# Optimization experiments

Hardware: AMD Instinct MI355X
Metric: run time of the kernel (lower is better)

Reference implementation:

```python
import jax, jax.numpy as jnp
import numpy as np

N_NEIGHBORS = 9
MIN_STD, MAX_STD = 0.01, 0.5
EPS_NORM = 1e-8


def setup_inputs() -> dict:
    key = jax.random.key(0)
    k1, k2, k3 = jax.random.split(key, 3)
    B, C, H, W = 8, 1024, 28, 28
    M, D = 16384, 1024
    features = jax.random.normal(k1, (B, C, H, W), dtype=jnp.float32)
    memory_bank = jax.random.normal(k2, (M, D), dtype=jnp.float32)
    influence_weight = jnp.ones((D,), dtype=jnp.float32)
    distance_weight = jnp.ones((1,), dtype=jnp.float32)
    eps = jax.random.normal(k3, (B * H * W, D), dtype=jnp.float32)  # randn_like noise
    return {"features": features, "memory_bank": memory_bank,
            "influence_weight": influence_weight, "distance_weight": distance_weight,
            "eps": eps}


def reference(features, memory_bank, influence_weight, distance_weight, eps):
    B, C, H, W = features.shape
    M, D = memory_bank.shape
    x = features.transpose(0, 2, 3, 1).reshape(B * H * W, C)  # [N, D]
    N = x.shape[0]

    d2 = (jnp.sum(x * x, axis=1, keepdims=True)
          + jnp.sum(memory_bank * memory_bank, axis=1)[None, :]
          - 2.0 * (x @ memory_bank.T))  # [N, M]
    dist = jnp.sqrt(jnp.clip(d2, 1e-12))

    k = min(N_NEIGHBORS, M)
    neg_topd, idx = jax.lax.top_k(-dist, k)  # smallest-k distances
    topk_distances = -neg_topd  # [N, k]

    # Per-dimension influence: mean |x - nn| over k neighbors, scaled by weight
    nn_feats = memory_bank[idx]  # [N, k, D] gather
    influence = jnp.abs(x[:, None, :] - nn_feats).mean(axis=1) * influence_weight[None, :]  # [N, D]

    # Row-wise normalization (torch std is unbiased, ddof=1)
    infl_norm = ((influence - influence.mean(axis=-1, keepdims=True))
                 / (jnp.std(influence, axis=-1, ddof=1, keepdims=True) + EPS_NORM))

    # Distance signal: per-row mean distance, normalized by global stats of the
    # [N, D]-expanded tensor (each row value repeated D times -> same mean,
    # unbiased std uses N*D - 1 in the denominator).
    ds = topk_distances.mean(axis=-1, keepdims=True)  # [N, 1]
    full_mean = ds.mean()
    full_std = jnp.sqrt(jnp.sum((ds - full_mean) ** 2) * D / (N * D - 1))
    dist_norm = (ds - full_mean) / (full_std + EPS_NORM)  # [N, 1], broadcasts over D

    combined = infl_norm + distance_weight * dist_norm  # [N, D]
    noise_std = MIN_STD + (MAX_STD - MIN_STD) * jax.nn.sigmoid(combined)

    noised = (x + eps * noise_std).reshape(B, H, W, C).transpose(0, 3, 1, 2)
    influence_map = influence.mean(axis=-1).reshape(B, H, W)
    noise_std_map = noise_std.mean(axis=-1).reshape(B, H, W)
    return noised, influence_map, noise_std_map
```

## Files before the change

kernel.cpp:

```cpp
#include <hip/hip_runtime.h>
#include <hip/hip_bf16.h>
#include <stdint.h>

#define N_ROWS 6272
#define DIM    1024
#define M_ROWS 16384
#define KNN    9
#define BMS    128
#define BNS    128
#define NPANEL 128
#define TOPC   6
#define NCAND  (NPANEL * 2 * TOPC)
#define TRR    16
#define LSTR   160

typedef __attribute__((ext_vector_type(4))) float f32x4;
typedef __attribute__((ext_vector_type(4))) int   i32x4;
typedef __attribute__((ext_vector_type(16))) int  i32x16;

#define QSCALE 31.75f

__device__ __forceinline__ int quant8(float v) {
  return __float2int_rn(fminf(fmaxf(v, -4.f), 4.f) * QSCALE);
}

__device__ __forceinline__ int kswz(int row, int col) {
  return col ^ ((row & 7) << 2) ^ (((row >> 3) & 1) << 5);
}

__global__ void k_prep_x(const float* __restrict__ feat,
                         float* __restrict__ xf, signed char* __restrict__ xq,
                         double* __restrict__ stats) {
  if (blockIdx.x == 0 && threadIdx.x < 2) stats[threadIdx.x] = 0.0;
  __shared__ float tile[32][33];
  const int ct = blockIdx.x & 31, nt = blockIdx.x >> 5;
  const int c0 = ct * 32, n0 = nt * 32;
  const int tx = threadIdx.x & 31, ty = threadIdx.x >> 5;
  {
    const int n = n0 + tx;
    const int b = n / 784, hw = n % 784;
    const float* src = feat + (size_t)b * 802816 + hw;
#pragma unroll
    for (int q = 0; q < 4; ++q)
      tile[ty + q * 8][tx] = src[(size_t)(c0 + ty + q * 8) * 784];
  }
  __syncthreads();
#pragma unroll
  for (int q = 0; q < 4; ++q) {
    const int nn = n0 + ty + q * 8;
    const int cc = c0 + tx;
    const float v = tile[tx][ty + q * 8];
    xf[(size_t)nn * DIM + cc] = v;
    xq[(size_t)nn * DIM + cc] = (signed char)quant8(v);
  }
}

__global__ void k_prep_m(const float* __restrict__ mb,
                         signed char* __restrict__ mq, int* __restrict__ mni) {
  const int j = blockIdx.x;
  const int t = threadIdx.x;
  const float* src = mb + (size_t)j * DIM;
  signed char* dst = mq + (size_t)j * DIM;
  int s = 0;
  for (int c = t; c < DIM; c += 256) {
    const int q = quant8(src[c]);
    dst[c] = (signed char)q;
    s += q * q;
  }
  __shared__ int red[4];
#pragma unroll
  for (int o = 32; o >= 1; o >>= 1) s += __shfl_down(s, o);
  if ((t & 63) == 0) red[t >> 6] = s;
  __syncthreads();
  if (t == 0) mni[j] = red[0] + red[1] + red[2] + red[3];
}

__launch_bounds__(256, 2)
__global__ void k_score(const signed char* __restrict__ xq,
                        const signed char* __restrict__ mq,
                        const int* __restrict__ mni,
                        unsigned int* __restrict__ cand) {
  __shared__ signed char S[81920];
  int* Kbuf = (int*)S;

  const int bx = blockIdx.x;
  const int xcd = bx & 7, i = bx >> 3;
  const int panel = i & 15, agroup = i >> 4;
  const int j0 = xcd * 2048 + panel * BNS;
  const int pglob = xcd * 16 + panel;

  const int t = threadIdx.x;
  const int lane = t & 63, w = t >> 6;
  const int wr = w >> 1, wc = w & 1;
  const int l31 = lane & 31, kh = lane >> 5;

  int srcOff[4], ldsOff[4];
#pragma unroll
  for (int cpy = 0; cpy < 4; ++cpy) {
    const int c = cpy * 256 + t;
    const int row = c >> 3, s = c & 7;
    srcOff[cpy] = row * DIM + s * 16;
    ldsOff[cpy] = row * LSTR + ((s ^ (row & 7)) << 4);
  }
  const signed char* bBase = mq + (size_t)j0 * DIM;

  int mn_[2];
#pragma unroll
  for (int ni = 0; ni < 2; ++ni) mn_[ni] = mni[j0 + wc * 64 + ni * 32 + l31];

  const int tcount = (agroup == 0) ? 13 : 12;
#pragma unroll 1
  for (int k7 = 0; k7 < tcount; ++k7) {
    const int tile = agroup + 4 * k7;
    const int r0 = tile * BMS;
    const signed char* aBase = xq + (size_t)r0 * DIM;

    i32x16 acc[2][2];
#pragma unroll
    for (int mi = 0; mi < 2; ++mi)
#pragma unroll
      for (int ni = 0; ni < 2; ++ni)
#pragma unroll
        for (int r = 0; r < 16; ++r) acc[mi][ni][r] = 0;

    i32x4 ra[4], rb[4];
#pragma unroll
    for (int cpy = 0; cpy < 4; ++cpy) {
      ra[cpy] = *(const i32x4*)(aBase + srcOff[cpy]);
      rb[cpy] = *(const i32x4*)(bBase + srcOff[cpy]);
    }
#pragma unroll
    for (int cpy = 0; cpy < 4; ++cpy) {
      *(i32x4*)(S + ldsOff[cpy]) = ra[cpy];
      *(i32x4*)(S + 40960 + ldsOff[cpy]) = rb[cpy];
    }
    asm volatile("s_waitcnt lgkmcnt(0)" ::: "memory");
    __builtin_amdgcn_s_barrier();

#pragma unroll 1
    for (int kt = 0; kt < 8; ++kt) {
      const int cb = (kt & 1) * 20480;
      const signed char* Ab = S + cb;
      const signed char* Bb = S + 40960 + cb;
      if (kt < 7) {
        const int kk = (kt + 1) * 128;
#pragma unroll
        for (int cpy = 0; cpy < 4; ++cpy) {
          ra[cpy] = *(const i32x4*)(aBase + srcOff[cpy] + kk);
          rb[cpy] = *(const i32x4*)(bBase + srcOff[cpy] + kk);
        }
      }
      __builtin_amdgcn_s_setprio(1);
#pragma unroll
      for (int ks = 0; ks < 4; ++ks) {
        const int sr = 2 * ks + kh;
        i32x4 a[2], b[2];
#pragma unroll
        for (int mi = 0; mi < 2; ++mi) {
          const int r = wr * 64 + mi * 32 + l31;
          a[mi] = *(const i32x4*)(Ab + r * LSTR + ((sr ^ (r & 7)) << 4));
        }
#pragma unroll
        for (int ni = 0; ni < 2; ++ni) {
          const int r = wc * 64 + ni * 32 + l31;
          b[ni] = *(const i32x4*)(Bb + r * LSTR + ((sr ^ (r & 7)) << 4));
        }
#pragma unroll
        for (int mi = 0; mi < 2; ++mi)
#pragma unroll
          for (int ni = 0; ni < 2; ++ni)
            acc[mi][ni] = __builtin_amdgcn_mfma_i32_32x32x32_i8(a[mi], b[ni], acc[mi][ni], 0, 0, 0);
      }
      __builtin_amdgcn_s_setprio(0);
      if (kt < 7) {
        const int nb = ((kt + 1) & 1) * 20480;
#pragma unroll
        for (int cpy = 0; cpy < 4; ++cpy) {
          *(i32x4*)(S + nb + ldsOff[cpy]) = ra[cpy];
          *(i32x4*)(S + 40960 + nb + ldsOff[cpy]) = rb[cpy];
        }
      }
      asm volatile("s_waitcnt lgkmcnt(0)" ::: "memory");
      __builtin_amdgcn_s_barrier();
    }

#pragma unroll
    for (int mi = 0; mi < 2; ++mi)
#pragma unroll
      for (int ni = 0; ni < 2; ++ni) {
        const int col = wc * 64 + ni * 32 + l31;
        const int mn = mn_[ni];
#pragma unroll
        for (int r = 0; r < 16; ++r) {
          const int row = wr * 64 + mi * 32 + 4 * kh + (r & 3) + 8 * (r >> 2);
          Kbuf[row * 128 + kswz(row, col)] = mn - 2 * acc[mi][ni][r];
        }
      }
    __syncthreads();
    {
      const int row = t >> 1, half = t & 1;
      unsigned tk[TOPC];
#pragma unroll
      for (int s = 0; s < TOPC; ++s) tk[s] = 0xFFFFFFFFu;
#pragma unroll
      for (int q = 0; q < 16; ++q) {
        const int cl = half * 64 + q * 4;
        const i32x4 v = *(const i32x4*)(Kbuf + row * 128 + kswz(row, cl));
#pragma unroll
        for (int e = 0; e < 4; ++e) {
          const unsigned p = (((unsigned)(v[e] + (1 << 25)) >> 11) << 14)
                             | (unsigned)(j0 + cl + e);
          if (p < tk[0]) {
            tk[0] = p;
#pragma unroll
            for (int s = 0; s < TOPC - 1; ++s) {
              const unsigned hi = tk[s] > tk[s + 1] ? tk[s] : tk[s + 1];
              const unsigned lo = tk[s] > tk[s + 1] ? tk[s + 1] : tk[s];
              tk[s] = hi; tk[s + 1] = lo;
            }
          }
        }
      }
      const size_t base = (size_t)(r0 + row) * NCAND + (size_t)(pglob * 2 + half) * TOPC;
#pragma unroll
      for (int s = 0; s < TOPC; ++s) cand[base + s] = tk[s];
    }
    __syncthreads();
  }
}

__global__ void k_rerank(const float* __restrict__ xf, const float* __restrict__ mb,
                         const unsigned int* __restrict__ cand,
                         int* __restrict__ idx9, double* __restrict__ dsv,
                         double* __restrict__ stats) {
  const int n = blockIdx.x, t = threadIdx.x;
  __shared__ float    xs[DIM];
  __shared__ unsigned cs[NCAND];
  __shared__ unsigned sel[TRR];
  __shared__ double dpart[256];
  __shared__ double d2s[TRR];
  __shared__ double dist_s[TRR];
  __shared__ int    rank_s[TRR];

  const float* xrow = xf + (size_t)n * DIM;
  for (int c = t; c < DIM; c += 256) xs[c] = xrow[c];
  const size_t cb = (size_t)n * NCAND;
  for (int s = t; s < NCAND; s += 256) cs[s] = cand[cb + s];
  __syncthreads();

  if (t < 64) {
    unsigned ck[24];
#pragma unroll
    for (int s = 0; s < 24; ++s) ck[s] = cs[t + 64 * s];
    for (int it = 0; it < TRR; ++it) {
      unsigned best = ck[0];
#pragma unroll
      for (int s = 1; s < 24; ++s) best = best < ck[s] ? best : ck[s];
#pragma unroll
      for (int off = 32; off >= 1; off >>= 1) {
        const unsigned o = (unsigned)__shfl_xor((int)best, off);
        best = best < o ? best : o;
      }
      if (t == 0) sel[it] = best;
#pragma unroll
      for (int s = 0; s < 24; ++s) if (ck[s] == best) ck[s] = 0xFFFFFFFFu;
    }
  }
  __syncthreads();
  {
    const int s = t >> 4, l16 = t & 15;
    const int j = (int)(sel[s] & 16383u);
    const float* mrow = mb + (size_t)j * DIM;
    double a = 0.0;
    for (int i = 0; i < 64; ++i) {
      const int c = l16 + (i << 4);
      const double d = (double)xs[c] - (double)mrow[c];
      a += d * d;
    }
    dpart[t] = a;
  }
  __syncthreads();
  if (t < TRR) {
    double v = 0.0;
    for (int i = 0; i < 16; ++i) v += dpart[t * 16 + i];
    d2s[t] = v;
    dist_s[t] = sqrt(v < 1e-12 ? 1e-12 : v);
  }
  __syncthreads();
  if (t < TRR) {
    const double v = d2s[t]; const int id = (int)(sel[t] & 16383u);
    int r = 0;
    for (int u = 0; u < TRR; ++u) {
      const double vu = d2s[u];
      const int idu = (int)(sel[u] & 16383u);
      if (vu < v || (vu == v && idu < id)) ++r;
    }
    rank_s[t] = r;
    if (r < KNN) idx9[n * KNN + r] = id;
  }
  __syncthreads();
  if (t == 0) {
    double sum = 0.0;
    for (int u = 0; u < TRR; ++u) if (rank_s[u] < KNN) sum += dist_s[u];
    const double m9 = sum * (1.0 / KNN);
    dsv[n] = m9;
    atomicAdd(&stats[0], m9);
    atomicAdd(&stats[1], m9 * m9);
  }
}

__global__ void k_final_b(const float* __restrict__ xf, const float* __restrict__ mb,
                          const float* __restrict__ iw, const float* __restrict__ dwp,
                          const float* __restrict__ eps, const int* __restrict__ idx9,
                          const double* __restrict__ dsv, const double* __restrict__ stats,
                          float* __restrict__ tn, float* __restrict__ out) {
  const int n = blockIdx.x, t = threadIdx.x;
  __shared__ float xs[DIM];
  __shared__ int js[KNN];
  __shared__ float rs1[4], rs2[4];
  const float* xrow = xf + (size_t)n * DIM;
  for (int c = t; c < DIM; c += 256) xs[c] = xrow[c];
  if (t < KNN) js[t] = idx9[n * KNN + t];
  __syncthreads();

  float infl[4];
  float s1 = 0.f, s2 = 0.f;
#pragma unroll
  for (int q = 0; q < 4; ++q) {
    const int c = t + q * 256;
    const float x = xs[c];
    float a = 0.f;
#pragma unroll
    for (int k = 0; k < KNN; ++k) a += fabsf(x - mb[(size_t)js[k] * DIM + c]);
    const float v = a * (1.0f / KNN) * iw[c];
    infl[q] = v; s1 += v; s2 += v * v;
  }
#pragma unroll
  for (int o = 32; o >= 1; o >>= 1) { s1 += __shfl_down(s1, o); s2 += __shfl_down(s2, o); }
  if ((t & 63) == 0) { rs1[t >> 6] = s1; rs2[t >> 6] = s2; }
  __syncthreads();
  const float sum = rs1[0] + rs1[1] + rs1[2] + rs1[3];
  const float sq  = rs2[0] + rs2[1] + rs2[2] + rs2[3];
  const float mean = sum * (1.0f / DIM);
  float var = (sq - (float)DIM * mean * mean) * (1.0f / (DIM - 1));
  var = fmaxf(var, 0.f);
  const float inv = 1.0f / (sqrtf(var) + 1e-8f);

  const double S1 = stats[0], S2 = stats[1];
  const double meanD = S1 / (double)N_ROWS;
  double varTop = S2 - S1 * S1 / (double)N_ROWS;
  if (varTop < 0.0) varTop = 0.0;
  const double fullstd = sqrt(varTop * (double)DIM / ((double)N_ROWS * DIM - 1.0)) + 1e-8;
  const float dn = (float)((dsv[n] - meanD) / fullstd);
  const float zb = dwp[0] * dn;

  float* trow = tn + (size_t)n * DIM;
  const float* ep = eps + (size_t)n * DIM;
  float si = 0.f, sn = 0.f;
#pragma unroll
  for (int q = 0; q < 4; ++q) {
    const int c = t + q * 256;
    const float v = infl[q];
    const float z = (v - mean) * inv + zb;
    const float ns = 0.01f + 0.49f / (1.0f + expf(-z));
    trow[c] = xs[c] + ep[c] * ns;
    si += v; sn += ns;
  }
  __syncthreads();
#pragma unroll
  for (int o = 32; o >= 1; o >>= 1) { si += __shfl_down(si, o); sn += __shfl_down(sn, o); }
  if ((t & 63) == 0) { rs1[t >> 6] = si; rs2[t >> 6] = sn; }
  __syncthreads();
  if (t == 0) {
    out[6422528 + n]        = (rs1[0] + rs1[1] + rs1[2] + rs1[3]) * (1.0f / DIM);
    out[6422528 + 6272 + n] = (rs2[0] + rs2[1] + rs2[2] + rs2[3]) * (1.0f / DIM);
  }
}

__global__ void k_tr(const float* __restrict__ tn, float* __restrict__ out) {
  __shared__ float tile[32][33];
  const int ct = blockIdx.x & 31, nt = blockIdx.x >> 5;
  const int c0 = ct * 32, n0 = nt * 32;
  const int tx = threadIdx.x & 31, ty = threadIdx.x >> 5;
#pragma unroll
  for (int q = 0; q < 4; ++q)
    tile[ty + q * 8][tx] = tn[(size_t)(n0 + ty + q * 8) * DIM + c0 + tx];
  __syncthreads();
  const int n = n0 + tx;
  const int b = n / 784, hw = n % 784;
  float* dst = out + (size_t)b * 802816 + hw;
#pragma unroll
  for (int q = 0; q < 4; ++q)
    dst[(size_t)(c0 + ty + q * 8) * 784] = tile[tx][ty + q * 8];
}

extern "C" void kernel_launch(void* const* d_in, const int* in_sizes, int n_in,
                              void* d_out, int out_size, void* d_ws, size_t ws_size,
                              hipStream_t stream) {
  (void)in_sizes; (void)n_in; (void)out_size; (void)ws_size;
  const float* feat = (const float*)d_in[0];
  const float* mb   = (const float*)d_in[1];
  const float* iw   = (const float*)d_in[2];
  const float* dw   = (const float*)d_in[3];
  const float* eps  = (const float*)d_in[4];
  float* out = (float*)d_out;

  char* p = (char*)d_ws;
  float* xf = (float*)p;                     p += (size_t)N_ROWS * DIM * 4;
  signed char* xq = (signed char*)p;         p += (size_t)N_ROWS * DIM;
  signed char* mq = (signed char*)p;         p += (size_t)M_ROWS * DIM;
  int* mni = (int*)p;                        p += (size_t)M_ROWS * 4;
  unsigned int* cand = (unsigned int*)p;     p += (size_t)N_ROWS * NCAND * 4;
  int* idx9 = (int*)p;                       p += (size_t)N_ROWS * KNN * 4;
  p = (char*)(((uintptr_t)p + 255) & ~(uintptr_t)255);
  double* dsv = (double*)p;                  p += (size_t)N_ROWS * 8;
  double* stats = (double*)p;                p += 64;
  float* tn = (float*)cand;

  k_prep_x<<<6272, 256, 0, stream>>>(feat, xf, xq, stats);
  k_prep_m<<<M_ROWS, 256, 0, stream>>>(mb, mq, mni);
  k_score<<<512, 256, 0, stream>>>(xq, mq, mni, cand);
  k_rerank<<<N_ROWS, 256, 0, stream>>>(xf, mb, cand, idx9, dsv, stats);
  k_final_b<<<N_ROWS, 256, 0, stream>>>(xf, mb, iw, dw, eps, idx9, dsv, stats, tn, out);
  k_tr<<<6272, 256, 0, stream>>>(tn, out);
}
```

Baseline: 435.4 us.

## Early-reject top-k candidates by threshold, remap threads, fuse transpose into final kernel

In the scoring kernel, each thread now keeps a running integer threshold derived from its current worst kept candidate. It skips packing and the insertion network for scores that cannot enter the top set. The row/half mapping also changes so consecutive threads read consecutive rows. The final kernel now writes noised values straight into the NCHW output with a 784-element stride, which removes the temporary buffer and the separate transpose kernel but makes those stores uncoalesced.

```diff
diff --git a/kernel.cpp b/kernel.cpp
--- a/kernel.cpp
+++ b/kernel.cpp
@@ -198,25 +198,29 @@
       }
     __syncthreads();
     {
-      const int row = t >> 1, half = t & 1;
+      const int row = t & 127, half = t >> 7;
       unsigned tk[TOPC];
 #pragma unroll
       for (int s = 0; s < TOPC; ++s) tk[s] = 0xFFFFFFFFu;
+      int thr = 0x7FFFFFFF;
 #pragma unroll
       for (int q = 0; q < 16; ++q) {
         const int cl = half * 64 + q * 4;
         const i32x4 v = *(const i32x4*)(Kbuf + row * 128 + kswz(row, cl));
 #pragma unroll
         for (int e = 0; e < 4; ++e) {
-          const unsigned p = (((unsigned)(v[e] + (1 << 25)) >> 11) << 14)
-                             | (unsigned)(j0 + cl + e);
-          if (p < tk[0]) {
-            tk[0] = p;
-#pragma unroll
-            for (int s = 0; s < TOPC - 1; ++s) {
-              const unsigned hi = tk[s] > tk[s + 1] ? tk[s] : tk[s + 1];
-              const unsigned lo = tk[s] > tk[s + 1] ? tk[s + 1] : tk[s];
-              tk[s] = hi; tk[s + 1] = lo;
+          if (v[e] < thr) {
+            const unsigned p = (((unsigned)(v[e] + (1 << 25)) >> 11) << 14)
+                               | (unsigned)(j0 + cl + e);
+            if (p < tk[0]) {
+              tk[0] = p;
+#pragma unroll
+              for (int s = 0; s < TOPC - 1; ++s) {
+                const unsigned hi = tk[s] > tk[s + 1] ? tk[s] : tk[s + 1];
+                const unsigned lo = tk[s] > tk[s + 1] ? tk[s + 1] : tk[s];
+                tk[s] = hi; tk[s + 1] = lo;
+              }
+              thr = (int)(((tk[0] >> 14) + 1u) << 11) - (1 << 25);
             }
           }
         }
@@ -309,11 +313,11 @@
   }
 }
 
-__global__ void k_final_b(const float* __restrict__ xf, const float* __restrict__ mb,
-                          const float* __restrict__ iw, const float* __restrict__ dwp,
-                          const float* __restrict__ eps, const int* __restrict__ idx9,
-                          const double* __restrict__ dsv, const double* __restrict__ stats,
-                          float* __restrict__ tn, float* __restrict__ out) {
+__global__ void k_final(const float* __restrict__ xf, const float* __restrict__ mb,
+                        const float* __restrict__ iw, const float* __restrict__ dwp,
+                        const float* __restrict__ eps, const int* __restrict__ idx9,
+                        const double* __restrict__ dsv, const double* __restrict__ stats,
+                        float* __restrict__ out) {
   const int n = blockIdx.x, t = threadIdx.x;
   __shared__ float xs[DIM];
   __shared__ int js[KNN];
@@ -354,7 +358,8 @@
   const float dn = (float)((dsv[n] - meanD) / fullstd);
   const float zb = dwp[0] * dn;
 
-  float* trow = tn + (size_t)n * DIM;
+  const int b = n / 784, hw = n % 784;
+  float* op = out + (size_t)b * 802816 + hw;
   const float* ep = eps + (size_t)n * DIM;
   float si = 0.f, sn = 0.f;
 #pragma unroll
@@ -363,7 +368,7 @@
     const float v = infl[q];
     const float z = (v - mean) * inv + zb;
     const float ns = 0.01f + 0.49f / (1.0f + expf(-z));
-    trow[c] = xs[c] + ep[c] * ns;
+    op[(size_t)c * 784] = xs[c] + ep[c] * ns;
     si += v; sn += ns;
   }
   __syncthreads();
@@ -375,23 +380,6 @@
     out[6422528 + n]        = (rs1[0] + rs1[1] + rs1[2] + rs1[3]) * (1.0f / DIM);
     out[6422528 + 6272 + n] = (rs2[0] + rs2[1] + rs2[2] + rs2[3]) * (1.0f / DIM);
   }
-}
-
-__global__ void k_tr(const float* __restrict__ tn, float* __restrict__ out) {
-  __shared__ float tile[32][33];
-  const int ct = blockIdx.x & 31, nt = blockIdx.x >> 5;
-  const int c0 = ct * 32, n0 = nt * 32;
-  const int tx = threadIdx.x & 31, ty = threadIdx.x >> 5;
-#pragma unroll
-  for (int q = 0; q < 4; ++q)
-    tile[ty + q * 8][tx] = tn[(size_t)(n0 + ty + q * 8) * DIM + c0 + tx];
-  __syncthreads();
-  const int n = n0 + tx;
-  const int b = n / 784, hw = n % 784;
-  float* dst = out + (size_t)b * 802816 + hw;
-#pragma unroll
-  for (int q = 0; q < 4; ++q)
-    dst[(size_t)(c0 + ty + q * 8) * 784] = tile[tx][ty + q * 8];
 }
 
 extern "C" void kernel_launch(void* const* d_in, const int* in_sizes, int n_in,
@@ -415,12 +403,10 @@
   p = (char*)(((uintptr_t)p + 255) & ~(uintptr_t)255);
   double* dsv = (double*)p;                  p += (size_t)N_ROWS * 8;
   double* stats = (double*)p;                p += 64;
-  float* tn = (float*)cand;
 
   k_prep_x<<<6272, 256, 0, stream>>>(feat, xf, xq, stats);
   k_prep_m<<<M_ROWS, 256, 0, stream>>>(mb, mq, mni);
   k_score<<<512, 256, 0, stream>>>(xq, mq, mni, cand);
   k_rerank<<<N_ROWS, 256, 0, stream>>>(xf, mb, cand, idx9, dsv, stats);
-  k_final_b<<<N_ROWS, 256, 0, stream>>>(xf, mb, iw, dw, eps, idx9, dsv, stats, tn, out);
-  k_tr<<<6272, 256, 0, stream>>>(tn, out);
-}
+  k_final<<<N_ROWS, 256, 0, stream>>>(xf, mb, iw, dw, eps, idx9, dsv, stats, out);
+}
```

Result: slower. 516.1 us (+18.5%).
